# Kernel optimization log

Hardware: AMD Instinct MI355X
Metric: run time of the kernel (lower is better)

Reference implementation:

```python
import jax, jax.numpy as jnp
import numpy as np

START_IDX = 1  # PAD_IDX = 0, END_IDX = 2 (unused in teacher-forcing path)
B, N, F = 16, 49, 1024
H, E, V = 1024, 1024, 15000
S, W = 5, 12


def setup_inputs() -> dict:
    key = jax.random.key(0)
    ks = jax.random.split(key, 16)
    def w(k, shape, s=0.02):
        return jax.random.normal(k, shape, dtype=jnp.float32) * s
    emb = w(ks[0], (V, E)).at[0].set(0.0)  # padding_idx = 0
    return dict(
        features=jax.random.normal(ks[1], (B, N, F), dtype=jnp.float32),
        reports=jax.random.randint(ks[2], (B, S, W), 0, V),
        attn_w1=w(ks[3], (F + H, H)), attn_b1=jnp.zeros((H,), jnp.float32),
        attn_w2=w(ks[4], (H, 1)), attn_b2=jnp.zeros((1,), jnp.float32),
        s_wih=w(ks[5], (4 * H, F)), s_whh=w(ks[6], (4 * H, H)),
        s_bih=jnp.zeros((4 * H,), jnp.float32), s_bhh=jnp.zeros((4 * H,), jnp.float32),
        stop_w=w(ks[7], (H, 1)), stop_b=jnp.zeros((1,), jnp.float32),
        emb=emb,
        w_wih=w(ks[8], (4 * H, E)), w_whh=w(ks[9], (4 * H, H)),
        w_bih=jnp.zeros((4 * H,), jnp.float32), w_bhh=jnp.zeros((4 * H,), jnp.float32),
        fc_w=w(ks[10], (H, V)), fc_b=jnp.zeros((V,), jnp.float32),
    )


def _lstm_cell(x, h, c, wih, whh, bih, bhh):
    # PyTorch LSTMCell: gates ordered i, f, g, o
    gates = x @ wih.T + h @ whh.T + (bih + bhh)
    i, f, g, o = jnp.split(gates, 4, axis=-1)
    c = jax.nn.sigmoid(f) * c + jax.nn.sigmoid(i) * jnp.tanh(g)
    h = jax.nn.sigmoid(o) * jnp.tanh(c)
    return h, c


def _attention(features, h, w1, b1, w2, b2):
    # features [B,N,F], h [B,H] -> additive 2-layer attention over N locations
    b, n, _ = features.shape
    hcat = jnp.broadcast_to(h[:, None, :], (b, n, h.shape[-1]))
    x = jnp.concatenate([features, hcat], axis=-1)           # [B,N,F+H]
    e = (jnp.tanh(x @ w1 + b1) @ w2 + b2)[..., 0]            # [B,N]
    scores = jax.nn.softmax(e, axis=-1)
    att = jnp.einsum('bn,bnf->bf', scores, features)          # [B,F]
    return att, scores


def _forward(features, reports, attn_w1, attn_b1, attn_w2, attn_b2,
             s_wih, s_whh, s_bih, s_bhh, stop_w, stop_b, emb,
             w_wih, w_whh, w_bih, w_bhh, fc_w, fc_b):
    bsz = features.shape[0]
    h0 = jnp.zeros((bsz, s_whh.shape[-1]), features.dtype)
    att0, _ = _attention(features, h0, attn_w1, attn_b1, attn_w2, attn_b2)
    start_emb = jnp.broadcast_to(emb[START_IDX][None, :], (bsz, emb.shape[-1]))

    def sentence_step(carry, reports_i):   # reports_i: [W, B] teacher-forcing tokens
        h, c, att = carry
        h, c = _lstm_cell(att, h, c, s_wih, s_whh, s_bih, s_bhh)
        czero = jnp.zeros_like(h)

        def word_step(wc, idx):
            hw, cw, inp = wc
            hw, cw = _lstm_cell(inp, hw, cw, w_wih, w_whh, w_bih, w_bhh)
            pred = hw @ fc_w + fc_b                           # [B,V]
            return (hw, cw, emb[idx]), pred

        # word LSTM initialized with h=topic, c=0; first input = <start> embedding
        _, preds = jax.lax.scan(word_step, (h, czero, start_emb), reports_i)  # [W,B,V]
        stop = jax.nn.sigmoid(h @ stop_w + stop_b)[:, 0]      # [B]
        att, scores = _attention(features, h, attn_w1, attn_b1, attn_w2, attn_b2)
        return (h, c, att), (preds, stop, scores)

    reports_sw = jnp.transpose(reports, (1, 2, 0))            # [S,W,B]
    _, (seq, stops, scores) = jax.lax.scan(sentence_step, (h0, h0, att0), reports_sw)
    seq_out = jnp.transpose(seq, (2, 0, 1, 3))                # [B,S,W,V]
    stops_out = jnp.transpose(stops, (1, 0))                  # [B,S]
    scores_out = jnp.transpose(scores, (1, 0, 2))             # [B,S,N]
    return seq_out, stops_out, scores_out


def reference(features, reports, attn_w1, attn_b1, attn_w2, attn_b2,
              s_wih, s_whh, s_bih, s_bhh, stop_w, stop_b, emb,
              w_wih, w_whh, w_bih, w_bhh, fc_w, fc_b):
    return _forward(features, reports, attn_w1, attn_b1, attn_w2, attn_b2,
                    s_wih, s_whh, s_bih, s_bhh, stop_w, stop_b, emb,
                    w_wih, w_whh, w_bih, w_bhh, fc_w, fc_b)
```

## Files before the change

kernel.cpp:

```cpp
#include <hip/hip_runtime.h>
#include <hip/hip_bf16.h>

#define B_  16
#define S_  5
#define W_  12
#define NL_ 49
#define H_  1024
#define V_  15000
#define SEQ_N   14400000
#define STOP_N  80
#define OUT_STOP (SEQ_N)
#define OUT_SCORE (SEQ_N + STOP_N)

typedef __attribute__((ext_vector_type(8))) short     short8;
typedef __attribute__((ext_vector_type(4))) float     f32x4;
typedef __attribute__((ext_vector_type(4))) unsigned int u32x4;
typedef __attribute__((ext_vector_type(4))) unsigned short us4;

#define OFF_FCWT   0ull
#define OFF_WWHHP  30720000ull
#define OFF_WWIHP  39108608ull
#define OFF_WSCATP 47497216ull
#define OFF_W1AT   64274432ull
#define OFF_W1BT   66371584ull
#define OFF_FBF    68468736ull
#define OFF_XIN    70074368ull
#define OFF_PF     72040448ull
#define OFF_XW     75251712ull
#define OFF_HBALL  90980352ull
#define OFF_HWBF0  92946432ull
#define OFF_HWBF1  93110272ull
#define OFF_ACAT1  93274112ull
#define OFF_H      93339648ull
#define OFF_EVAL   93405184ull
#define OFF_ACAT0  93408384ull
#define OFF_C      93473920ull
#define OFF_CW     93539456ull
#define OFF_HPROJ  93867136ull
#define WS_TOTAL   93932672ull
#define ZERO_BASE  OFF_ACAT0
#define ZERO_BYTES (524288ull)

__device__ __forceinline__ unsigned short f2bf(float x){
  unsigned u = __float_as_uint(x);
  u += 0x7fffu + ((u >> 16) & 1u);
  return (unsigned short)(u >> 16);
}
__device__ __forceinline__ float sigm(float x){ return 1.f/(1.f+expf(-x)); }

typedef __attribute__((address_space(3))) unsigned int  as3_u32;
typedef __attribute__((address_space(1))) const unsigned int as1_u32;

__device__ __forceinline__ void gl16(const void* g, void* l){
  __builtin_amdgcn_global_load_lds((as1_u32*)g, (as3_u32*)l, 16, 0, 0);
}

template<int ROWS,int CH,int NW>
__device__ __forceinline__ void stage_swz(const unsigned short* __restrict__ gbase, int grs,
                                          unsigned short* lds, int wid, int lane,
                                          int r0, int rmax){
  constexpr int RPI = 64/CH;
  constexpr int NISS = ROWS/RPI;
  const int r_in = lane / CH;
  const int cbp  = lane % CH;
  #pragma unroll
  for (int it = wid; it < NISS; it += NW){
    int rl = it*RPI + r_in;
    int gr = r0 + rl; gr = gr < rmax ? gr : rmax-1;
    int cb = cbp ^ (rl & 7);
    gl16(gbase + (size_t)gr*grs + cb*8, lds + it*RPI*CH*8);
  }
}

__device__ __forceinline__ void transp64(const float* __restrict__ src, int sld,
                                         int rb, int cb, int Cc,
                                         unsigned short* __restrict__ dst, int dld,
                                         float (*t)[65])
{
  const int tx = threadIdx.x & 15, ty = threadIdx.x >> 4;
  #pragma unroll
  for (int ii = 0; ii < 4; ii++){
    int r = ty + ii*16;
    int c = cb + tx*4;
    const float* s = src + (size_t)(rb + r)*sld + c;
    f32x4 v;
    if (c + 4 <= Cc) v = *(const f32x4*)s;
    else {
      v[0] = (c   < Cc) ? s[0] : 0.f;
      v[1] = (c+1 < Cc) ? s[1] : 0.f;
      v[2] = (c+2 < Cc) ? s[2] : 0.f;
      v[3] = (c+3 < Cc) ? s[3] : 0.f;
    }
    t[r][tx*4+0]=v[0]; t[r][tx*4+1]=v[1]; t[r][tx*4+2]=v[2]; t[r][tx*4+3]=v[3];
  }
  __syncthreads();
  #pragma unroll
  for (int ii = 0; ii < 4; ii++){
    int c = ty + ii*16;
    if (cb + c < Cc){
      int r4 = tx*4;
      us4 o; o[0]=f2bf(t[r4][c]); o[1]=f2bf(t[r4+1][c]); o[2]=f2bf(t[r4+2][c]); o[3]=f2bf(t[r4+3][c]);
      *(us4*)(dst + (size_t)(cb + c)*dld + rb + r4) = o;
    }
  }
}

#define U0 200704u
#define U1 (U0+1048576u)
#define U2 (U1+1048576u)
#define U3 (U2+1048576u)
#define U4 (U3+1048576u)
#define U5 (U4+245760u)
#define NCVT_BLK 1280
#define NTR_BLK  2136
#define NZ_BLK   16
#define NPREP    (NCVT_BLK + NTR_BLK + NZ_BLK)

__device__ __forceinline__ void cvt_gate_unit(const float* __restrict__ src,
                                              unsigned short* __restrict__ dst,
                                              unsigned e, int dld, int doff){
  int n = e >> 8, cc = (e & 255)*4;
  int gate = (n >> 4) & 3, j = ((n >> 6) << 4) | (n & 15);
  f32x4 v = *(const f32x4*)(src + ((size_t)(gate*1024 + j) << 10) + cc);
  us4 o; o[0]=f2bf(v[0]); o[1]=f2bf(v[1]); o[2]=f2bf(v[2]); o[3]=f2bf(v[3]);
  *(us4*)(dst + (size_t)n*dld + doff + cc) = o;
}

__global__ void k_prep(const float* __restrict__ features,
                       const float* __restrict__ w_whh, const float* __restrict__ w_wih,
                       const float* __restrict__ s_wih, const float* __restrict__ s_whh,
                       const float* __restrict__ emb, const int* __restrict__ reports,
                       const float* __restrict__ attn_w1, const float* __restrict__ fc_w,
                       unsigned short* __restrict__ FBF, unsigned short* __restrict__ WWHHP,
                       unsigned short* __restrict__ WWIHP, unsigned short* __restrict__ WSCATP,
                       unsigned short* __restrict__ XIN,
                       unsigned short* __restrict__ W1AT, unsigned short* __restrict__ W1BT,
                       unsigned short* __restrict__ FCWT, char* __restrict__ zbase)
{
  __shared__ float t[64][65];
  int bx = blockIdx.x;
  if (bx < NCVT_BLK){
    for (unsigned u = bx*256u + threadIdx.x; u < U5; u += NCVT_BLK*256u){
      if (u < U0){
        int idx = u*4;
        f32x4 v = *(const f32x4*)(features + idx);
        us4 o; o[0]=f2bf(v[0]); o[1]=f2bf(v[1]); o[2]=f2bf(v[2]); o[3]=f2bf(v[3]);
        *(us4*)(FBF + idx) = o;
      } else if (u < U1){
        cvt_gate_unit(w_whh, WWHHP, u - U0, 1024, 0);
      } else if (u < U2){
        cvt_gate_unit(w_wih, WWIHP, u - U1, 1024, 0);
      } else if (u < U3){
        cvt_gate_unit(s_wih, WSCATP, u - U2, 2048, 0);
      } else if (u < U4){
        cvt_gate_unit(s_whh, WSCATP, u - U3, 2048, 1024);
      } else {
        unsigned e = u - U4;
        int m = e >> 8, k = (e & 255)*4;
        int w = m / 80, r = m % 80, s = r >> 4, b = r & 15;
        int tok = (w == 0) ? 1 : reports[b*60 + s*12 + (w-1)];
        f32x4 v = *(const f32x4*)(emb + ((size_t)tok << 10) + k);
        us4 o; o[0]=f2bf(v[0]); o[1]=f2bf(v[1]); o[2]=f2bf(v[2]); o[3]=f2bf(v[3]);
        *(us4*)(XIN + (size_t)m*1024 + k) = o;
      }
    }
  } else if (bx < NCVT_BLK + NTR_BLK){
    int base = (bx - NCVT_BLK)*2;
    #pragma unroll
    for (int bt = 0; bt < 2; bt++){
      if (bt) __syncthreads();
      int tile = base + bt;
      if (tile < 512){
        int z = tile >> 8, rem = tile & 255;
        int rb = (rem & 15)*64, cb = (rem >> 4)*64;
        transp64(attn_w1 + (size_t)z*1024*1024, 1024, rb, cb, 1024, z ? W1BT : W1AT, 1024, t);
      } else {
        int ft = tile - 512;
        int rb = (ft & 15)*64, cb = (ft >> 4)*64;
        transp64(fc_w, V_, rb, cb, V_, FCWT, 1024, t);
      }
    }
  } else {
    int idx = bx - (NCVT_BLK + NTR_BLK);
    #pragma unroll
    for (int it = 0; it < 8; it++){
      size_t off = ((size_t)(idx + it*NZ_BLK))*4096 + threadIdx.x*16;
      *(u32x4*)(zbase + off) = (u32x4){0u,0u,0u,0u};
    }
  }
}

template<int BM,int BN,int BK,int WM,int WN,int EPI>
__global__ void k_gemm(const unsigned short* __restrict__ A, int lda,
                       const unsigned short* __restrict__ Bt, int ldb,
                       float* __restrict__ C, int ldc,
                       const float* __restrict__ bias,
                       int M, int N, int K)
{
  constexpr int NWV = WM*WN;
  constexpr int CH = BK/8;
  __shared__ __align__(16) unsigned short As[BM*BK];
  __shared__ __align__(16) unsigned short Bs[BN*BK];
  const int n0 = blockIdx.x * BN, m0 = blockIdx.y * BM;
  if (n0 >= N) return;
  const int tid  = threadIdx.x;
  const int lane = tid & 63;
  const int wave = tid >> 6;
  constexpr int WROWS = BM/WM, WCOLS = BN/WN;
  constexpr int FM = WROWS/16, FN = WCOLS/16;
  const int wm = wave / WN, wn = wave % WN;
  const int g = lane >> 4, fr = lane & 15;
  const int sx = fr & 7;

  f32x4 acc[FM][FN];
  #pragma unroll
  for (int a=0;a<FM;a++)
    #pragma unroll
    for (int b=0;b<FN;b++) acc[a][b] = (f32x4){0.f,0.f,0.f,0.f};

  for (int k0 = 0; k0 < K; k0 += BK) {
    if (k0) __syncthreads();
    stage_swz<BM,CH,NWV>(A + k0, lda, As, wave, lane, m0, M);
    stage_swz<BN,CH,NWV>(Bt + k0, ldb, Bs, wave, lane, n0, N);
    __syncthreads();
    #pragma unroll
    for (int kk = 0; kk < BK; kk += 32) {
      const int so = ((kk/8 + g) ^ sx) * 8;
      short8 af[FM], bt[FN];
      #pragma unroll
      for (int fm=0; fm<FM; fm++)
        af[fm] = *(const short8*)(As + (wm*WROWS + fm*16 + fr)*BK + so);
      #pragma unroll
      for (int fn=0; fn<FN; fn++)
        bt[fn] = *(const short8*)(Bs + (wn*WCOLS + fn*16 + fr)*BK + so);
      #pragma unroll
      for (int fm=0; fm<FM; fm++)
        #pragma unroll
        for (int fn=0; fn<FN; fn++)
          acc[fm][fn] = __builtin_amdgcn_mfma_f32_16x16x32_bf16(af[fm], bt[fn], acc[fm][fn], 0, 0, 0);
    }
  }

  #pragma unroll
  for (int fm=0; fm<FM; fm++)
    #pragma unroll
    for (int fn=0; fn<FN; fn++)
      #pragma unroll
      for (int j=0; j<4; j++){
        int m = m0 + wm*WROWS + fm*16 + g*4 + j;
        int n = n0 + wn*WCOLS + fn*16 + fr;
        if (m < M && n < N) {
          float v = acc[fm][fn][j];
          if (EPI == 1 || EPI == 2) v += bias[n];
          if (EPI == 2) {
            int b = m & 15, s = (m >> 4) % 5, w = m / 80;
            __builtin_nontemporal_store(v, &C[(size_t)((b*5 + s)*12 + w)*V_ + n]);
          } else if (EPI == 3) {
            __builtin_nontemporal_store(v, &C[(size_t)m*ldc + n]);
          } else {
            C[(size_t)m*ldc + n] = v;
          }
        }
      }
}

template<int BM,int BN,int BK,int WN,int SENT>
__global__ void k_gemm_cell(const unsigned short* __restrict__ A, int lda,
                            const unsigned short* __restrict__ Bt, int ldb,
                            const float* __restrict__ Xg, int ldx,
                            const float* __restrict__ bih, const float* __restrict__ bhh,
                            float* __restrict__ cst,
                            unsigned short* __restrict__ h1, int ldh1,
                            unsigned short* __restrict__ h2,
                            float* __restrict__ hf,
                            int M, int K)
{
  constexpr int CH = BK/8;
  __shared__ __align__(16) unsigned short As[BM*BK];
  __shared__ __align__(16) unsigned short Bs[BN*BK];
  const int tid  = threadIdx.x;
  const int lane = tid & 63;
  const int wn   = tid >> 6;
  const int n0 = blockIdx.x * BN, m0 = blockIdx.y * BM;
  const int g = lane >> 4, fr = lane & 15;
  const int sx = fr & 7;

  f32x4 acc[4];
  #pragma unroll
  for (int b=0;b<4;b++) acc[b] = (f32x4){0.f,0.f,0.f,0.f};

  for (int k0 = 0; k0 < K; k0 += BK) {
    if (k0) __syncthreads();
    stage_swz<BM,CH,WN>(A + k0, lda, As, wn, lane, m0, M);
    stage_swz<BN,CH,WN>(Bt + k0, ldb, Bs, wn, lane, n0, 4096);
    __syncthreads();
    #pragma unroll
    for (int kk = 0; kk < BK; kk += 32) {
      const int so = ((kk/8 + g) ^ sx) * 8;
      short8 af = *(const short8*)(As + fr*BK + so);
      #pragma unroll
      for (int fn=0; fn<4; fn++){
        short8 bt = *(const short8*)(Bs + (wn*64 + fn*16 + fr)*BK + so);
        acc[fn] = __builtin_amdgcn_mfma_f32_16x16x32_bf16(af, bt, acc[fn], 0, 0, 0);
      }
    }
  }

  const int nb = n0 + wn*64 + fr;
  const int j  = ((n0 + wn*64) >> 2) + fr;
  const float b0 = bih[j]        + bhh[j];
  const float b1 = bih[1024 + j] + bhh[1024 + j];
  const float b2 = bih[2048 + j] + bhh[2048 + j];
  const float b3 = bih[3072 + j] + bhh[3072 + j];
  #pragma unroll
  for (int jj=0; jj<4; jj++){
    int m = m0 + g*4 + jj;
    if (m < M){
      float gi = acc[0][jj] + b0;
      float gf = acc[1][jj] + b1;
      float gg = acc[2][jj] + b2;
      float go = acc[3][jj] + b3;
      if (!SENT){
        const float* xg = Xg + (size_t)m*ldx + nb;
        gi += xg[0]; gf += xg[16]; gg += xg[32]; go += xg[48];
      }
      float cn = sigm(gf)*cst[m*1024 + j] + sigm(gi)*tanhf(gg);
      float hn = sigm(go)*tanhf(cn);
      cst[m*1024 + j] = cn;
      unsigned short hb = f2bf(hn);
      h1[(size_t)m*ldh1 + j] = hb;
      h2[(size_t)m*1024 + j] = hb;
      if (SENT) hf[m*1024 + j] = hn;
    }
  }
}

__global__ void k_attn_e(const float* __restrict__ PF, const float* __restrict__ hproj,
                         const float* __restrict__ w2, float* __restrict__ evals)
{
  const int bn = blockIdx.x;
  const int b  = bn / NL_;
  const int tid = threadIdx.x;
  __shared__ float red[4];
  const float* pf = PF + ((size_t)bn << 10);
  const float* hp = hproj + (b << 10);
  int k = tid * 4;
  f32x4 a = *(const f32x4*)(pf + k);
  f32x4 hh = *(const f32x4*)(hp + k);
  f32x4 w = *(const f32x4*)(w2 + k);
  float p = tanhf(a[0]+hh[0])*w[0] + tanhf(a[1]+hh[1])*w[1]
          + tanhf(a[2]+hh[2])*w[2] + tanhf(a[3]+hh[3])*w[3];
  #pragma unroll
  for (int o = 32; o; o >>= 1) p += __shfl_down(p, o, 64);
  if ((tid & 63) == 0) red[tid >> 6] = p;
  __syncthreads();
  if (tid == 0) evals[bn] = red[0] + red[1] + red[2] + red[3];
}

template<int INIT>
__global__ void k_attn_fin(const float* __restrict__ evals, const float* __restrict__ features,
                           const float* __restrict__ h, const float* __restrict__ stop_w,
                           const float* __restrict__ stop_b,
                           unsigned short* __restrict__ Acat, float* __restrict__ outp, int s)
{
  const int b = blockIdx.x, tid = threadIdx.x;
  __shared__ float scs[64];
  __shared__ float red[4];
  if (tid < 64){
    float e = (tid < NL_) ? evals[b*NL_ + tid] : -1e30f;
    float mx = e;
    #pragma unroll
    for (int o = 32; o; o >>= 1) mx = fmaxf(mx, __shfl_xor(mx, o, 64));
    float ex = (tid < NL_) ? expf(e - mx) : 0.f;
    float dn = ex;
    #pragma unroll
    for (int o = 32; o; o >>= 1) dn += __shfl_xor(dn, o, 64);
    float sc = ex / dn;
    if (tid < NL_){
      scs[tid] = sc;
      if (!INIT) outp[OUT_SCORE + (b*5 + s)*NL_ + tid] = sc;
    }
  }
  __syncthreads();
  {
    int f0 = tid * 4;
    f32x4 a = (f32x4){0.f,0.f,0.f,0.f};
    const float* fb = features + (((size_t)b*NL_) << 10) + f0;
    #pragma unroll 7
    for (int n = 0; n < NL_; n++){
      f32x4 v = *(const f32x4*)(fb + ((size_t)n << 10));
      float sc = scs[n];
      a[0] += sc*v[0]; a[1] += sc*v[1]; a[2] += sc*v[2]; a[3] += sc*v[3];
    }
    us4 o4; o4[0]=f2bf(a[0]); o4[1]=f2bf(a[1]); o4[2]=f2bf(a[2]); o4[3]=f2bf(a[3]);
    *(us4*)(Acat + b*2048 + f0) = o4;
  }
  if (!INIT){
    int k = tid * 4;
    f32x4 hv = *(const f32x4*)(h + (b << 10) + k);
    f32x4 sw = *(const f32x4*)(stop_w + k);
    float p = hv[0]*sw[0] + hv[1]*sw[1] + hv[2]*sw[2] + hv[3]*sw[3];
    #pragma unroll
    for (int o = 32; o; o >>= 1) p += __shfl_down(p, o, 64);
    if ((tid & 63) == 0) red[tid >> 6] = p;
    __syncthreads();
    if (tid == 0) outp[OUT_STOP + b*5 + s] = sigm(red[0]+red[1]+red[2]+red[3] + stop_b[0]);
  }
}

extern "C" void kernel_launch(void* const* d_in, const int* in_sizes, int n_in,
                              void* d_out, int out_size, void* d_ws, size_t ws_size,
                              hipStream_t stream)
{
  const float* features = (const float*)d_in[0];
  const int*   reports  = (const int*)d_in[1];
  const float* attn_w1  = (const float*)d_in[2];
  const float* attn_b1  = (const float*)d_in[3];
  const float* attn_w2  = (const float*)d_in[4];
  const float* s_wih    = (const float*)d_in[6];
  const float* s_whh    = (const float*)d_in[7];
  const float* s_bih    = (const float*)d_in[8];
  const float* s_bhh    = (const float*)d_in[9];
  const float* stop_w   = (const float*)d_in[10];
  const float* stop_b   = (const float*)d_in[11];
  const float* emb      = (const float*)d_in[12];
  const float* w_wih    = (const float*)d_in[13];
  const float* w_whh    = (const float*)d_in[14];
  const float* w_bih    = (const float*)d_in[15];
  const float* w_bhh    = (const float*)d_in[16];
  const float* fc_w     = (const float*)d_in[17];
  const float* fc_b     = (const float*)d_in[18];
  float* out = (float*)d_out;
  char*  ws  = (char*)d_ws;
  if (ws_size < WS_TOTAL) return;

  unsigned short* FCWT   = (unsigned short*)(ws + OFF_FCWT);
  unsigned short* WWHHP  = (unsigned short*)(ws + OFF_WWHHP);
  unsigned short* WWIHP  = (unsigned short*)(ws + OFF_WWIHP);
  unsigned short* WSCATP = (unsigned short*)(ws + OFF_WSCATP);
  unsigned short* W1AT   = (unsigned short*)(ws + OFF_W1AT);
  unsigned short* W1BT   = (unsigned short*)(ws + OFF_W1BT);
  unsigned short* FBF    = (unsigned short*)(ws + OFF_FBF);
  unsigned short* XIN    = (unsigned short*)(ws + OFF_XIN);
  float*          PF     = (float*)(ws + OFF_PF);
  float*          XW     = (float*)(ws + OFF_XW);
  unsigned short* HBALL  = (unsigned short*)(ws + OFF_HBALL);
  unsigned short* HW0    = (unsigned short*)(ws + OFF_HWBF0);
  unsigned short* HW1    = (unsigned short*)(ws + OFF_HWBF1);
  unsigned short* ACAT0  = (unsigned short*)(ws + OFF_ACAT0);
  unsigned short* ACAT1  = (unsigned short*)(ws + OFF_ACAT1);
  float*          Hst    = (float*)(ws + OFF_H);
  float*          Cst    = (float*)(ws + OFF_C);
  float*          CW     = (float*)(ws + OFF_CW);
  float*          HPROJ  = (float*)(ws + OFF_HPROJ);
  float*          EVAL   = (float*)(ws + OFF_EVAL);

  k_prep<<<NPREP, 256, 0, stream>>>(features, w_whh, w_wih, s_wih, s_whh, emb, reports,
                                    attn_w1, fc_w,
                                    FBF, WWHHP, WWIHP, WSCATP, XIN, W1AT, W1BT, FCWT,
                                    ws + ZERO_BASE);

  k_gemm<64,64,128,2,2,1><<<dim3(16,13), 256, 0, stream>>>(FBF,1024, W1AT,1024, PF,1024, attn_b1, 784,1024,1024);
  k_gemm<64,128,128,2,2,3><<<dim3(32,15), 256, 0, stream>>>(XIN,1024, WWIHP,1024, XW,4096, nullptr, 960,4096,1024);

  k_attn_e<<<784, 256, 0, stream>>>(PF, HPROJ, attn_w2, EVAL);
  k_attn_fin<1><<<16, 256, 0, stream>>>(EVAL, features, Hst, stop_w, stop_b, ACAT0, out, 0);

  unsigned short* ACS[2] = {ACAT0, ACAT1};
  for (int s = 0; s < S_; s++){
    unsigned short* cur = ACS[s & 1];
    unsigned short* nxt = ACS[(s + 1) & 1];
    k_gemm_cell<16,128,256,2,1><<<dim3(32,1), 128, 0, stream>>>(
        cur, 2048, WSCATP, 2048, nullptr, 0, s_bih, s_bhh, Cst,
        nxt + 1024, 2048, HW0 + s*16*1024, Hst, 16, 2048);
    k_gemm<16,64,256,1,4,0><<<dim3(16,1), 256, 0, stream>>>(
        nxt + 1024, 2048, W1BT, 1024, HPROJ, 1024, nullptr, 16, 1024, 1024);
    k_attn_e<<<784, 256, 0, stream>>>(PF, HPROJ, attn_w2, EVAL);
    k_attn_fin<0><<<16, 256, 0, stream>>>(EVAL, features, Hst, stop_w, stop_b, nxt, out, s);
  }

  unsigned short* HW[2] = {HW0, HW1};
  for (int w = 0; w < W_; w++){
    k_gemm_cell<16,128,256,2,0><<<dim3(32,5), 128, 0, stream>>>(
        HW[w & 1], 1024, WWHHP, 1024, XW + (size_t)w*80*4096, 4096, w_bih, w_bhh, CW,
        HW[(w + 1) & 1], 1024, HBALL + (size_t)w*80*1024, nullptr, 80, 1024);
  }

  k_gemm<64,128,64,2,2,2><<<dim3(120,15), 256, 0, stream>>>(HBALL,1024, FCWT,1024, out,V_, fc_b, 960,15000,1024);
}
```

Measured before the change: 515.4 us.

## Fuse attention energy and finalize kernels via last-block atomic counter

Merges the attention energy kernel and the softmax/context/stop kernel into one launch. Each batch's 49 blocks bump an atomic counter, and the last one to arrive does the softmax, weighted feature sum and stop output, which saves a kernel launch and a dependency per sentence step. It also raises the K-tile of the LSTM cell GEMM from 256 to 512 and increases the prep conversion block count. The counter must be zeroed in prep and reset by the last block, and it adds fences and atomic traffic.

```diff
diff --git a/kernel.cpp b/kernel.cpp
--- a/kernel.cpp
+++ b/kernel.cpp
@@ -37,7 +37,8 @@
 #define OFF_C      93473920ull
 #define OFF_CW     93539456ull
 #define OFF_HPROJ  93867136ull
-#define WS_TOTAL   93932672ull
+#define OFF_CNT    93932672ull
+#define WS_TOTAL   93936768ull
 #define ZERO_BASE  OFF_ACAT0
 #define ZERO_BYTES (524288ull)
 
@@ -111,7 +112,7 @@
 #define U3 (U2+1048576u)
 #define U4 (U3+1048576u)
 #define U5 (U4+245760u)
-#define NCVT_BLK 1280
+#define NCVT_BLK 2048
 #define NTR_BLK  2136
 #define NZ_BLK   16
 #define NPREP    (NCVT_BLK + NTR_BLK + NZ_BLK)
@@ -187,6 +188,8 @@
       size_t off = ((size_t)(idx + it*NZ_BLK))*4096 + threadIdx.x*16;
       *(u32x4*)(zbase + off) = (u32x4){0u,0u,0u,0u};
     }
+    if (idx == 0)
+      *(u32x4*)(zbase + 524288 + threadIdx.x*16) = (u32x4){0u,0u,0u,0u};
   }
 }
 
@@ -335,39 +338,48 @@
   }
 }
 
-__global__ void k_attn_e(const float* __restrict__ PF, const float* __restrict__ hproj,
-                         const float* __restrict__ w2, float* __restrict__ evals)
+template<int INIT>
+__global__ void k_attn(const float* __restrict__ PF, const float* __restrict__ hproj,
+                       const float* __restrict__ w2, const float* __restrict__ features,
+                       const float* __restrict__ hF, const float* __restrict__ stop_w,
+                       const float* __restrict__ stop_b,
+                       float* __restrict__ evals, unsigned* __restrict__ cnt,
+                       unsigned short* __restrict__ Acat, float* __restrict__ outp, int s)
 {
   const int bn = blockIdx.x;
   const int b  = bn / NL_;
   const int tid = threadIdx.x;
   __shared__ float red[4];
-  const float* pf = PF + ((size_t)bn << 10);
-  const float* hp = hproj + (b << 10);
-  int k = tid * 4;
-  f32x4 a = *(const f32x4*)(pf + k);
-  f32x4 hh = *(const f32x4*)(hp + k);
-  f32x4 w = *(const f32x4*)(w2 + k);
-  float p = tanhf(a[0]+hh[0])*w[0] + tanhf(a[1]+hh[1])*w[1]
-          + tanhf(a[2]+hh[2])*w[2] + tanhf(a[3]+hh[3])*w[3];
-  #pragma unroll
-  for (int o = 32; o; o >>= 1) p += __shfl_down(p, o, 64);
-  if ((tid & 63) == 0) red[tid >> 6] = p;
+  __shared__ int last;
+  {
+    const float* pf = PF + ((size_t)bn << 10);
+    const float* hp = hproj + (b << 10);
+    int k = tid * 4;
+    f32x4 a = *(const f32x4*)(pf + k);
+    f32x4 hh = *(const f32x4*)(hp + k);
+    f32x4 w = *(const f32x4*)(w2 + k);
+    float p = tanhf(a[0]+hh[0])*w[0] + tanhf(a[1]+hh[1])*w[1]
+            + tanhf(a[2]+hh[2])*w[2] + tanhf(a[3]+hh[3])*w[3];
+    #pragma unroll
+    for (int o = 32; o; o >>= 1) p += __shfl_down(p, o, 64);
+    if ((tid & 63) == 0) red[tid >> 6] = p;
+    __syncthreads();
+    if (tid == 0) evals[bn] = red[0] + red[1] + red[2] + red[3];
+  }
+  if (tid == 0){
+    __threadfence();
+    unsigned old = atomicAdd(&cnt[b], 1u);
+    last = (old == NL_ - 1);
+  }
   __syncthreads();
-  if (tid == 0) evals[bn] = red[0] + red[1] + red[2] + red[3];
-}
-
-template<int INIT>
-__global__ void k_attn_fin(const float* __restrict__ evals, const float* __restrict__ features,
-                           const float* __restrict__ h, const float* __restrict__ stop_w,
-                           const float* __restrict__ stop_b,
-                           unsigned short* __restrict__ Acat, float* __restrict__ outp, int s)
-{
-  const int b = blockIdx.x, tid = threadIdx.x;
+  if (!last) return;
+  if (tid == 0) atomicExch(&cnt[b], 0u);
+  __threadfence();
   __shared__ float scs[64];
-  __shared__ float red[4];
   if (tid < 64){
-    float e = (tid < NL_) ? evals[b*NL_ + tid] : -1e30f;
+    float e = -1e30f;
+    if (tid < NL_)
+      e = __hip_atomic_load(&evals[b*NL_ + tid], __ATOMIC_RELAXED, __HIP_MEMORY_SCOPE_AGENT);
     float mx = e;
     #pragma unroll
     for (int o = 32; o; o >>= 1) mx = fmaxf(mx, __shfl_xor(mx, o, 64));
@@ -397,7 +409,7 @@
   }
   if (!INIT){
     int k = tid * 4;
-    f32x4 hv = *(const f32x4*)(h + (b << 10) + k);
+    f32x4 hv = *(const f32x4*)(hF + (b << 10) + k);
     f32x4 sw = *(const f32x4*)(stop_w + k);
     float p = hv[0]*sw[0] + hv[1]*sw[1] + hv[2]*sw[2] + hv[3]*sw[3];
     #pragma unroll
@@ -454,6 +466,7 @@
   float*          CW     = (float*)(ws + OFF_CW);
   float*          HPROJ  = (float*)(ws + OFF_HPROJ);
   float*          EVAL   = (float*)(ws + OFF_EVAL);
+  unsigned*       CNT    = (unsigned*)(ws + OFF_CNT);
 
   k_prep<<<NPREP, 256, 0, stream>>>(features, w_whh, w_wih, s_wih, s_whh, emb, reports,
                                     attn_w1, fc_w,
@@ -463,25 +476,25 @@
   k_gemm<64,64,128,2,2,1><<<dim3(16,13), 256, 0, stream>>>(FBF,1024, W1AT,1024, PF,1024, attn_b1, 784,1024,1024);
   k_gemm<64,128,128,2,2,3><<<dim3(32,15), 256, 0, stream>>>(XIN,1024, WWIHP,1024, XW,4096, nullptr, 960,4096,1024);
 
-  k_attn_e<<<784, 256, 0, stream>>>(PF, HPROJ, attn_w2, EVAL);
-  k_attn_fin<1><<<16, 256, 0, stream>>>(EVAL, features, Hst, stop_w, stop_b, ACAT0, out, 0);
+  k_attn<1><<<784, 256, 0, stream>>>(PF, HPROJ, attn_w2, features, Hst, stop_w, stop_b,
+                                     EVAL, CNT, ACAT0, out, 0);
 
   unsigned short* ACS[2] = {ACAT0, ACAT1};
   for (int s = 0; s < S_; s++){
     unsigned short* cur = ACS[s & 1];
     unsigned short* nxt = ACS[(s + 1) & 1];
-    k_gemm_cell<16,128,256,2,1><<<dim3(32,1), 128, 0, stream>>>(
+    k_gemm_cell<16,128,512,2,1><<<dim3(32,1), 128, 0, stream>>>(
         cur, 2048, WSCATP, 2048, nullptr, 0, s_bih, s_bhh, Cst,
         nxt + 1024, 2048, HW0 + s*16*1024, Hst, 16, 2048);
     k_gemm<16,64,256,1,4,0><<<dim3(16,1), 256, 0, stream>>>(
         nxt + 1024, 2048, W1BT, 1024, HPROJ, 1024, nullptr, 16, 1024, 1024);
-    k_attn_e<<<784, 256, 0, stream>>>(PF, HPROJ, attn_w2, EVAL);
-    k_attn_fin<0><<<16, 256, 0, stream>>>(EVAL, features, Hst, stop_w, stop_b, nxt, out, s);
+    k_attn<0><<<784, 256, 0, stream>>>(PF, HPROJ, attn_w2, features, Hst, stop_w, stop_b,
+                                       EVAL, CNT, nxt, out, s);
   }
 
   unsigned short* HW[2] = {HW0, HW1};
   for (int w = 0; w < W_; w++){
-    k_gemm_cell<16,128,256,2,0><<<dim3(32,5), 128, 0, stream>>>(
+    k_gemm_cell<16,128,512,2,0><<<dim3(32,5), 128, 0, stream>>>(
         HW[w & 1], 1024, WWHHP, 1024, XW + (size_t)w*80*4096, 4096, w_bih, w_bhh, CW,
         HW[(w + 1) & 1], 1024, HBALL + (size_t)w*80*1024, nullptr, 80, 1024);
   }
```

Measured after the change: 632.1 us. 1.23x slower.
